# Kernel tuning notes

Measured on AMD Instinct MI355X. Metric: run time of the kernel, lower is better.

Reference implementation:

```python
import jax, jax.numpy as jnp
import numpy as np

B, N, D = 8, 1024, 1024
H, DH = 16, 64
INNER = H * DH  # == D by construction
MLP = 4096
EPS = 1e-5


def layernorm(x, g, b):
    mu = jnp.mean(x, axis=-1, keepdims=True)
    var = jnp.mean(jnp.square(x - mu), axis=-1, keepdims=True)
    return (x - mu) * jax.lax.rsqrt(var + EPS) * g + b


def setup_inputs() -> dict:
    key = jax.random.key(0)
    ks = jax.random.split(key, 10)
    s = lambda fan_in: 1.0 / np.sqrt(fan_in)
    return {
        "x": jax.random.normal(ks[0], (B, N, D), jnp.float32),
        "ln1_g": jnp.ones((D,), jnp.float32),
        "ln1_b": jnp.zeros((D,), jnp.float32),
        "w_qkv": jax.random.uniform(ks[1], (D, 3 * INNER), jnp.float32, -s(D), s(D)),
        "w_out": jax.random.uniform(ks[2], (INNER, D), jnp.float32, -s(INNER), s(INNER)),
        "b_out": jnp.zeros((D,), jnp.float32),
        "ln2_g": jnp.ones((D,), jnp.float32),
        "ln2_b": jnp.zeros((D,), jnp.float32),
        "w1": jax.random.uniform(ks[3], (D, MLP), jnp.float32, -s(D), s(D)),
        "b1": jnp.zeros((MLP,), jnp.float32),
        "w2": jax.random.uniform(ks[4], (MLP, D), jnp.float32, -s(MLP), s(MLP)),
        "b2": jnp.zeros((D,), jnp.float32),
    }


def reference(x, ln1_g, ln1_b, w_qkv, w_out, b_out, ln2_g, ln2_b, w1, b1, w2, b2):
    scale = DH ** -0.5
    xn = layernorm(x, ln1_g, ln1_b)
    qkv = xn @ w_qkv  # [B, N, 3*INNER]
    embed_dim = xn.shape[-1]
    # faithful to source: slice by embed_dim (== INNER here)
    q, k, v = (qkv[:, :, embed_dim * i: embed_dim * (i + 1)] for i in range(3))
    reshape_heads = lambda t: t.reshape(B, N, H, DH).transpose(0, 2, 1, 3)  # b h n d
    q, k, v = reshape_heads(q), reshape_heads(k), reshape_heads(v)
    scores = jnp.einsum("bhnd,bhmd->bhnm", q, k) * scale
    attn = jax.nn.softmax(scores, axis=-1)
    attn_out = jnp.einsum("bhnm,bhmd->bhnd", attn, v)
    attn_out = attn_out.transpose(0, 2, 1, 3).reshape(B, N, INNER)
    x2 = attn_out @ w_out + b_out  # to_ff projection (project_out=True)
    # feed_forward: LayerNorm -> Linear -> GELU(exact) -> Linear (dropout=0)
    h = layernorm(x2, ln2_g, ln2_b) @ w1 + b1
    h = jax.nn.gelu(h, approximate=False)
    out = h @ w2 + b2
    return out
```

## Files before the change

kernel.cpp:

```cpp
#include <hip/hip_runtime.h>
#include <hip/hip_bf16.h>
#include <math.h>

typedef __bf16 bf16;
typedef __bf16 bf16x8 __attribute__((ext_vector_type(8)));
typedef float f32x4 __attribute__((ext_vector_type(4)));

#define SEQ 1024
#define DMODEL 1024

__global__ void transpose_f2b(const float* __restrict__ in, bf16* __restrict__ out,
                              int K, int N) {
    __shared__ float tile[32][33];
    int n0 = blockIdx.x * 32, k0 = blockIdx.y * 32;
    int tx = threadIdx.x, ty = threadIdx.y;
#pragma unroll
    for (int i = 0; i < 4; ++i) {
        int kk = ty + i * 8;
        tile[kk][tx] = in[(size_t)(k0 + kk) * N + n0 + tx];
    }
    __syncthreads();
#pragma unroll
    for (int i = 0; i < 4; ++i) {
        int nn = ty + i * 8;
        out[(size_t)(n0 + nn) * K + k0 + tx] = (bf16)tile[tx][nn];
    }
}

__global__ void ln_f2b(const float* __restrict__ x, const float* __restrict__ g,
                       const float* __restrict__ bta, bf16* __restrict__ y) {
    int row = blockIdx.x, t = threadIdx.x;
    const float* xr = x + (size_t)row * DMODEL;
    float v[4];
#pragma unroll
    for (int i = 0; i < 4; ++i) v[i] = xr[t * 4 + i];
    float s = v[0] + v[1] + v[2] + v[3];
    float s2 = v[0] * v[0] + v[1] * v[1] + v[2] * v[2] + v[3] * v[3];
#pragma unroll
    for (int off = 32; off > 0; off >>= 1) {
        s += __shfl_down(s, off, 64);
        s2 += __shfl_down(s2, off, 64);
    }
    __shared__ float ws1[4], ws2[4];
    __shared__ float mu_s, rstd_s;
    int lane = t & 63, wv = t >> 6;
    if (lane == 0) { ws1[wv] = s; ws2[wv] = s2; }
    __syncthreads();
    if (t == 0) {
        float S1 = ws1[0] + ws1[1] + ws1[2] + ws1[3];
        float S2 = ws2[0] + ws2[1] + ws2[2] + ws2[3];
        float mu = S1 * (1.0f / DMODEL);
        float var = S2 * (1.0f / DMODEL) - mu * mu;
        mu_s = mu;
        rstd_s = rsqrtf(var + 1e-5f);
    }
    __syncthreads();
    float mu = mu_s, rstd = rstd_s;
    bf16* yr = y + (size_t)row * DMODEL;
#pragma unroll
    for (int i = 0; i < 4; ++i) {
        int d = t * 4 + i;
        float o = (v[i] - mu) * rstd * g[d] + bta[d];
        yr[d] = (bf16)o;
    }
}

#define BM 128
#define BN 128
#define BK 32
#define LDT 40

__global__ __launch_bounds__(256, 2) void gemm_bt(
    const bf16* __restrict__ A, const bf16* __restrict__ Bt,
    const float* __restrict__ bias, void* __restrict__ Cv,
    int M, int N, int K, int mode) {
    __shared__ bf16 sA[BM][LDT];
    __shared__ bf16 sB[BN][LDT];
    int t = threadIdx.x;
    int lane = t & 63, wave = t >> 6;
    int wr = wave >> 1, wc = wave & 1;
    int m0 = blockIdx.y * BM, n0 = blockIdx.x * BN;
    int ar = t >> 2;
    int ak = (t & 3) * 8;
    const bf16* Ap = A + (size_t)m0 * K;
    const bf16* Bp = Bt + (size_t)n0 * K;

    f32x4 acc[4][4];
#pragma unroll
    for (int i = 0; i < 4; ++i)
#pragma unroll
        for (int j = 0; j < 4; ++j) acc[i][j] = (f32x4){0.f, 0.f, 0.f, 0.f};

    int mq = lane & 15, kq = (lane >> 4) * 8;

    for (int k0 = 0; k0 < K; k0 += BK) {
        __syncthreads();
        *(uint4*)&sA[ar][ak]      = *(const uint4*)(Ap + (size_t)ar * K + k0 + ak);
        *(uint4*)&sA[ar + 64][ak] = *(const uint4*)(Ap + (size_t)(ar + 64) * K + k0 + ak);
        *(uint4*)&sB[ar][ak]      = *(const uint4*)(Bp + (size_t)ar * K + k0 + ak);
        *(uint4*)&sB[ar + 64][ak] = *(const uint4*)(Bp + (size_t)(ar + 64) * K + k0 + ak);
        __syncthreads();
        bf16x8 af[4], bfr[4];
#pragma unroll
        for (int i = 0; i < 4; ++i)
            af[i] = *(const bf16x8*)&sA[wr * 64 + i * 16 + mq][kq];
#pragma unroll
        for (int j = 0; j < 4; ++j)
            bfr[j] = *(const bf16x8*)&sB[wc * 64 + j * 16 + mq][kq];
#pragma unroll
        for (int i = 0; i < 4; ++i)
#pragma unroll
            for (int j = 0; j < 4; ++j)
                acc[i][j] = __builtin_amdgcn_mfma_f32_16x16x32_bf16(af[i], bfr[j], acc[i][j], 0, 0, 0);
    }

    int cq = lane & 15, rq = (lane >> 4) * 4;
#pragma unroll
    for (int i = 0; i < 4; ++i) {
        int row = m0 + wr * 64 + i * 16 + rq;
#pragma unroll
        for (int j = 0; j < 4; ++j) {
            int col = n0 + wc * 64 + j * 16 + cq;
            float bv = bias ? bias[col] : 0.0f;
#pragma unroll
            for (int r = 0; r < 4; ++r) {
                float v = acc[i][j][r] + bv;
                if (mode == 1) v = 0.5f * v * (1.0f + erff(v * 0.70710678118654752f));
                size_t idx = (size_t)(row + r) * N + col;
                if (mode == 2) ((float*)Cv)[idx] = v;
                else           ((bf16*)Cv)[idx] = (bf16)v;
            }
        }
    }
}

#define LDK 72

__global__ __launch_bounds__(256, 2) void attn_mfma(const bf16* __restrict__ qkv,
                                                    bf16* __restrict__ ao) {
    __shared__ bf16 Klds[64][LDK];
    __shared__ bf16 Vtlds[64][LDK];
    __shared__ bf16 Plds[4][16][LDK];
    int t = threadIdx.x, lane = t & 63, wave = t >> 6;
    int bh = blockIdx.y, bb = bh >> 4, h = bh & 15;
    int q0 = blockIdx.x * 64;
    const bf16* base = qkv + (size_t)bb * SEQ * 3072;
    int m = lane & 15, quad = lane >> 4;
    int kq = quad * 8;

    bf16x8 qf[2];
    {
        int qrow = q0 + wave * 16 + m;
        const bf16* p = base + (size_t)qrow * 3072 + h * 64;
#pragma unroll
        for (int c = 0; c < 2; ++c) {
            bf16x8 tmp = *(const bf16x8*)(p + c * 32 + kq);
#pragma unroll
            for (int j = 0; j < 8; ++j) qf[c][j] = (bf16)((float)tmp[j] * 0.125f);
        }
    }

    float m_run[4], l_run[4];
    f32x4 o_acc[4];
#pragma unroll
    for (int r = 0; r < 4; ++r) { m_run[r] = -3e38f; l_run[r] = 0.f; }
#pragma unroll
    for (int g = 0; g < 4; ++g) o_acc[g] = (f32x4){0.f, 0.f, 0.f, 0.f};

    int skey = t >> 3, sd0 = (t & 7) * 8;

    for (int kt = 0; kt < 16; ++kt) {
        __syncthreads();
        {
            const bf16* pk = base + (size_t)(kt * 64 + skey) * 3072 + 1024 + h * 64 + sd0;
            *(bf16x8*)&Klds[skey][sd0]      = *(const bf16x8*)pk;
            *(bf16x8*)&Klds[skey + 32][sd0] = *(const bf16x8*)(pk + 32 * 3072);
            const bf16* pv = base + (size_t)(kt * 64 + skey) * 3072 + 2048 + h * 64 + sd0;
            bf16x8 v0 = *(const bf16x8*)pv;
            bf16x8 v1 = *(const bf16x8*)(pv + 32 * 3072);
#pragma unroll
            for (int i = 0; i < 8; ++i) {
                Vtlds[sd0 + i][skey]      = v0[i];
                Vtlds[sd0 + i][skey + 32] = v1[i];
            }
        }
        __syncthreads();

        f32x4 s[4];
#pragma unroll
        for (int g = 0; g < 4; ++g) {
            bf16x8 b0 = *(const bf16x8*)&Klds[g * 16 + m][kq];
            bf16x8 b1 = *(const bf16x8*)&Klds[g * 16 + m][32 + kq];
            s[g] = (f32x4){0.f, 0.f, 0.f, 0.f};
            s[g] = __builtin_amdgcn_mfma_f32_16x16x32_bf16(qf[0], b0, s[g], 0, 0, 0);
            s[g] = __builtin_amdgcn_mfma_f32_16x16x32_bf16(qf[1], b1, s[g], 0, 0, 0);
        }

#pragma unroll
        for (int r = 0; r < 4; ++r) {
            float mx = fmaxf(fmaxf(s[0][r], s[1][r]), fmaxf(s[2][r], s[3][r]));
#pragma unroll
            for (int msk = 1; msk < 16; msk <<= 1) mx = fmaxf(mx, __shfl_xor(mx, msk, 64));
            float m_new = fmaxf(m_run[r], mx);
            float alpha = __expf(m_run[r] - m_new);
            m_run[r] = m_new;
            float rowsum = 0.f;
#pragma unroll
            for (int g = 0; g < 4; ++g) {
                float p = __expf(s[g][r] - m_new);
                s[g][r] = p;
                rowsum += p;
            }
#pragma unroll
            for (int msk = 1; msk < 16; msk <<= 1) rowsum += __shfl_xor(rowsum, msk, 64);
            l_run[r] = l_run[r] * alpha + rowsum;
#pragma unroll
            for (int g = 0; g < 4; ++g) o_acc[g][r] *= alpha;
        }

#pragma unroll
        for (int g = 0; g < 4; ++g)
#pragma unroll
            for (int r = 0; r < 4; ++r)
                Plds[wave][quad * 4 + r][g * 16 + m] = (bf16)s[g][r];

#pragma unroll
        for (int kc = 0; kc < 2; ++kc) {
            bf16x8 pf = *(const bf16x8*)&Plds[wave][m][kc * 32 + kq];
#pragma unroll
            for (int dg = 0; dg < 4; ++dg) {
                bf16x8 vf = *(const bf16x8*)&Vtlds[dg * 16 + m][kc * 32 + kq];
                o_acc[dg] = __builtin_amdgcn_mfma_f32_16x16x32_bf16(pf, vf, o_acc[dg], 0, 0, 0);
            }
        }
    }

#pragma unroll
    for (int r = 0; r < 4; ++r) {
        int row = q0 + wave * 16 + quad * 4 + r;
        float rl = 1.0f / l_run[r];
        bf16* op = ao + ((size_t)bb * SEQ + row) * DMODEL + h * 64;
#pragma unroll
        for (int g = 0; g < 4; ++g) op[g * 16 + m] = (bf16)(o_acc[g][r] * rl);
    }
}

extern "C" void kernel_launch(void* const* d_in, const int* in_sizes, int n_in,
                              void* d_out, int out_size, void* d_ws, size_t ws_size,
                              hipStream_t stream) {
    const float* x     = (const float*)d_in[0];
    const float* ln1_g = (const float*)d_in[1];
    const float* ln1_b = (const float*)d_in[2];
    const float* w_qkv = (const float*)d_in[3];
    const float* w_out = (const float*)d_in[4];
    const float* b_out = (const float*)d_in[5];
    const float* ln2_g = (const float*)d_in[6];
    const float* ln2_b = (const float*)d_in[7];
    const float* w1    = (const float*)d_in[8];
    const float* b1    = (const float*)d_in[9];
    const float* w2    = (const float*)d_in[10];
    const float* b2    = (const float*)d_in[11];
    float* out = (float*)d_out;
    char* ws = (char*)d_ws;
    char* outc = (char*)d_out;

    bf16* wqkvT = (bf16*)(ws + (0ull << 20));
    bf16* woutT = (bf16*)(ws + (6ull << 20));
    bf16* qkv   = (bf16*)(ws + (8ull << 20));
    bf16* w1T   = (bf16*)(ws + (8ull << 20));
    bf16* w2T   = (bf16*)(ws + (16ull << 20));
    float* x2   = (float*)(ws + (24ull << 20));
    bf16* hbuf  = (bf16*)(ws + (24ull << 20));
    bf16* xn    = (bf16*)(outc + 0);
    bf16* ao    = (bf16*)(outc + 0);
    bf16* x2n   = (bf16*)(outc + (16ull << 20));

    dim3 tb(32, 8);
    transpose_f2b<<<dim3(3072 / 32, 1024 / 32), tb, 0, stream>>>(w_qkv, wqkvT, 1024, 3072);
    transpose_f2b<<<dim3(1024 / 32, 1024 / 32), tb, 0, stream>>>(w_out, woutT, 1024, 1024);

    ln_f2b<<<8192, 256, 0, stream>>>(x, ln1_g, ln1_b, xn);
    gemm_bt<<<dim3(3072 / 128, 8192 / 128), 256, 0, stream>>>(xn, wqkvT, nullptr, qkv,
                                                              8192, 3072, 1024, 0);
    attn_mfma<<<dim3(SEQ / 64, 128), 256, 0, stream>>>(qkv, ao);

    transpose_f2b<<<dim3(4096 / 32, 1024 / 32), tb, 0, stream>>>(w1, w1T, 1024, 4096);
    transpose_f2b<<<dim3(1024 / 32, 4096 / 32), tb, 0, stream>>>(w2, w2T, 4096, 1024);

    gemm_bt<<<dim3(1024 / 128, 8192 / 128), 256, 0, stream>>>(ao, woutT, b_out, x2,
                                                              8192, 1024, 1024, 2);
    ln_f2b<<<8192, 256, 0, stream>>>(x2, ln2_g, ln2_b, x2n);

    for (int c = 0; c < 2; ++c) {
        const bf16* a1 = x2n + (size_t)c * 4096 * 1024;
        float* oc = out + (size_t)c * 4096 * 1024;
        gemm_bt<<<dim3(4096 / 128, 4096 / 128), 256, 0, stream>>>(a1, w1T, b1, hbuf,
                                                                  4096, 4096, 1024, 1);
        gemm_bt<<<dim3(1024 / 128, 4096 / 128), 256, 0, stream>>>(hbuf, w2T, b2, oc,
                                                                  4096, 1024, 4096, 2);
    }
}
```

Before: 700.4 us.

## Load GEMM tiles via direct global-to-LDS with XOR swizzle; rotate V transpose writes

The GEMM tile loads now use global_load_lds to copy 16-byte chunks straight from global memory into LDS, skipping the trip through registers. An XOR swizzle on the chunk index replaces the padded LDS layout so fragment reads avoid bank conflicts. In the attention kernel, each thread's scattered V-transpose stores are issued in a rotated order to spread LDS bank accesses. The direct-to-LDS path depends on wave-contiguous destination layout, and getting the swizzle and addressing right is fiddly.

```diff
diff --git a/kernel.cpp b/kernel.cpp
--- a/kernel.cpp
+++ b/kernel.cpp
@@ -8,6 +8,12 @@
 
 #define SEQ 1024
 #define DMODEL 1024
+
+__device__ __forceinline__ void gld_lds16(const bf16* g, bf16* l) {
+    __builtin_amdgcn_global_load_lds(
+        (const __attribute__((address_space(1))) unsigned int*)g,
+        (__attribute__((address_space(3))) unsigned int*)l, 16, 0, 0);
+}
 
 __global__ void transpose_f2b(const float* __restrict__ in, bf16* __restrict__ out,
                               int K, int N) {
@@ -68,45 +74,55 @@
 #define BM 128
 #define BN 128
 #define BK 32
-#define LDT 40
 
 __global__ __launch_bounds__(256, 2) void gemm_bt(
     const bf16* __restrict__ A, const bf16* __restrict__ Bt,
     const float* __restrict__ bias, void* __restrict__ Cv,
     int M, int N, int K, int mode) {
-    __shared__ bf16 sA[BM][LDT];
-    __shared__ bf16 sB[BN][LDT];
+    __shared__ bf16 sA[BM * BK];
+    __shared__ bf16 sB[BN * BK];
     int t = threadIdx.x;
     int lane = t & 63, wave = t >> 6;
     int wr = wave >> 1, wc = wave & 1;
     int m0 = blockIdx.y * BM, n0 = blockIdx.x * BN;
-    int ar = t >> 2;
-    int ak = (t & 3) * 8;
     const bf16* Ap = A + (size_t)m0 * K;
     const bf16* Bp = Bt + (size_t)n0 * K;
 
+    int srow = wave * 16 + (lane >> 2);
+    int schunk = lane & 3;
+    int gcoff = (schunk ^ (srow & 3)) * 8;
+    const bf16* gA0 = Ap + (size_t)srow * K + gcoff;
+    const bf16* gA1 = Ap + (size_t)(srow + 64) * K + gcoff;
+    const bf16* gB0 = Bp + (size_t)srow * K + gcoff;
+    const bf16* gB1 = Bp + (size_t)(srow + 64) * K + gcoff;
+    bf16* lA0 = sA + wave * 512;
+    bf16* lA1 = sA + 2048 + wave * 512;
+    bf16* lB0 = sB + wave * 512;
+    bf16* lB1 = sB + 2048 + wave * 512;
+
     f32x4 acc[4][4];
 #pragma unroll
     for (int i = 0; i < 4; ++i)
 #pragma unroll
         for (int j = 0; j < 4; ++j) acc[i][j] = (f32x4){0.f, 0.f, 0.f, 0.f};
 
-    int mq = lane & 15, kq = (lane >> 4) * 8;
+    int mq = lane & 15, quad = lane >> 4;
+    int csw = (quad ^ (mq & 3)) * 8;
 
     for (int k0 = 0; k0 < K; k0 += BK) {
         __syncthreads();
-        *(uint4*)&sA[ar][ak]      = *(const uint4*)(Ap + (size_t)ar * K + k0 + ak);
-        *(uint4*)&sA[ar + 64][ak] = *(const uint4*)(Ap + (size_t)(ar + 64) * K + k0 + ak);
-        *(uint4*)&sB[ar][ak]      = *(const uint4*)(Bp + (size_t)ar * K + k0 + ak);
-        *(uint4*)&sB[ar + 64][ak] = *(const uint4*)(Bp + (size_t)(ar + 64) * K + k0 + ak);
+        gld_lds16(gA0 + k0, lA0);
+        gld_lds16(gA1 + k0, lA1);
+        gld_lds16(gB0 + k0, lB0);
+        gld_lds16(gB1 + k0, lB1);
         __syncthreads();
         bf16x8 af[4], bfr[4];
 #pragma unroll
         for (int i = 0; i < 4; ++i)
-            af[i] = *(const bf16x8*)&sA[wr * 64 + i * 16 + mq][kq];
+            af[i] = *(const bf16x8*)&sA[(wr * 64 + i * 16 + mq) * BK + csw];
 #pragma unroll
         for (int j = 0; j < 4; ++j)
-            bfr[j] = *(const bf16x8*)&sB[wc * 64 + j * 16 + mq][kq];
+            bfr[j] = *(const bf16x8*)&sB[(wc * 64 + j * 16 + mq) * BK + csw];
 #pragma unroll
         for (int i = 0; i < 4; ++i)
 #pragma unroll
@@ -168,6 +184,7 @@
     for (int g = 0; g < 4; ++g) o_acc[g] = (f32x4){0.f, 0.f, 0.f, 0.f};
 
     int skey = t >> 3, sd0 = (t & 7) * 8;
+    int rot = t & 7;
 
     for (int kt = 0; kt < 16; ++kt) {
         __syncthreads();
@@ -179,9 +196,10 @@
             bf16x8 v0 = *(const bf16x8*)pv;
             bf16x8 v1 = *(const bf16x8*)(pv + 32 * 3072);
 #pragma unroll
-            for (int i = 0; i < 8; ++i) {
-                Vtlds[sd0 + i][skey]      = v0[i];
-                Vtlds[sd0 + i][skey + 32] = v1[i];
+            for (int ii = 0; ii < 8; ++ii) {
+                int j = (ii + rot) & 7;
+                Vtlds[sd0 + j][skey]      = v0[j];
+                Vtlds[sd0 + j][skey + 32] = v1[j];
             }
         }
         __syncthreads();
```

After: 650.0 us. 7.2% less time.
